# Performance work log

Measured on AMD Instinct MI355X. Metric: run time of the kernel, lower is better.

## Reference

```python
import jax, jax.numpy as jnp
import numpy as np

DIM, HID = 1024, 2048
N_SHARED, N_ROUTED, TOP_K = 2, 6, 2
AUX_W = 0.01
B, T = 4, 2048


def _swiglu(x, w1, w2, w3):
    # x: [N, C]; w1,w3: [C, H]; w2: [H, C]
    return (jax.nn.silu(x @ w1) * (x @ w3)) @ w2


def setup_inputs() -> dict:
    key = jax.random.key(0)
    ks = jax.random.split(key, 9)
    s = 0.02
    return {
        "x": jax.random.normal(ks[0], (B, T, DIM), dtype=jnp.float32),
        "w1_s": jax.random.normal(ks[1], (N_SHARED, DIM, HID), dtype=jnp.float32) * s,
        "w2_s": jax.random.normal(ks[2], (N_SHARED, HID, DIM), dtype=jnp.float32) * s,
        "w3_s": jax.random.normal(ks[3], (N_SHARED, DIM, HID), dtype=jnp.float32) * s,
        "w1_r": jax.random.normal(ks[4], (N_ROUTED, DIM, HID), dtype=jnp.float32) * s,
        "w2_r": jax.random.normal(ks[5], (N_ROUTED, HID, DIM), dtype=jnp.float32) * s,
        "w3_r": jax.random.normal(ks[6], (N_ROUTED, DIM, HID), dtype=jnp.float32) * s,
        "gate_w": jax.random.normal(ks[7], (DIM, N_ROUTED), dtype=jnp.float32) * s,
        "out_w": jax.random.normal(ks[8], (DIM, DIM), dtype=jnp.float32) * s,
    }


def reference(x, w1_s, w2_s, w3_s, w1_r, w2_r, w3_r, gate_w, out_w):
    Bv, Tv, C = x.shape
    xf = x.reshape(-1, C)  # [N, C]

    # shared experts: always run for every token
    shared = jnp.zeros_like(xf)
    for e in range(N_SHARED):
        shared = shared + _swiglu(xf, w1_s[e], w2_s[e], w3_s[e])

    # router
    logits = xf @ gate_w                       # [N, E]
    wk, idx = jax.lax.top_k(logits, TOP_K)     # [N, K]
    wk = jax.nn.softmax(wk, axis=-1)           # softmax over selected k only

    # routed experts: dense per-expert pass scaled by (zero for unselected) weight
    routed = jnp.zeros_like(xf)
    for e in range(N_ROUTED):
        we = jnp.sum(wk * (idx == e).astype(xf.dtype), axis=-1, keepdims=True)  # [N,1]
        routed = routed + we * _swiglu(xf, w1_r[e], w2_r[e], w3_r[e])

    combined = shared + routed

    # aux load-balance loss (top-1 assignment fraction x mean prob)
    probs = jax.nn.softmax(logits, axis=-1)
    f_i = jnp.mean(jax.nn.one_hot(idx[:, 0], N_ROUTED, dtype=xf.dtype), axis=0)
    p_i = jnp.mean(probs, axis=0)
    aux_loss = AUX_W * N_ROUTED * jnp.sum(f_i * p_i)

    out = (combined @ out_w).reshape(Bv, Tv, C)
    return out, aux_loss
```

## Files before the change

### kernel.cpp

```cpp
#include <hip/hip_runtime.h>
#include <hip/hip_bf16.h>
#include <cstdint>

#define DIMc 1024
#define HIDc 2048
#define NTOK 8192
#define NRT 6

typedef __bf16 bf16x8 __attribute__((ext_vector_type(8)));
typedef __bf16 bf16x2v __attribute__((ext_vector_type(2)));
typedef float  f32x4  __attribute__((ext_vector_type(4)));

#define VMCNT(n) asm volatile("s_waitcnt vmcnt(" #n ")" ::: "memory")
#define RBAR()   asm volatile("s_barrier" ::: "memory")

__device__ __forceinline__ void gl_lds16(const void* gsrc, void* ldst) {
    auto g = (const __attribute__((address_space(1))) void*)gsrc;
    auto l = (__attribute__((address_space(3))) void*)ldst;
    __builtin_amdgcn_global_load_lds(g, l, 16, 0, 0);
}

__device__ __forceinline__ void xcd_swz(int lid, int nwg, int gx, int& bx, int& by) {
    int q = nwg >> 3, r = nwg & 7;
    int xcd = lid & 7, idx = lid >> 3;
    int nlid = (xcd < r ? xcd * (q + 1) : r * (q + 1) + (xcd - r) * q) + idx;
    bx = nlid % gx; by = nlid / gx;
}

__global__ __launch_bounds__(256) void tcvt_k(
    const float* __restrict__ w1s, const float* __restrict__ w2s, const float* __restrict__ w3s,
    const float* __restrict__ w1r, const float* __restrict__ w2r, const float* __restrict__ w3r,
    const float* __restrict__ outw,
    __bf16* __restrict__ W13T, __bf16* __restrict__ W2T, __bf16* __restrict__ OutWT)
{
    int id = blockIdx.z;
    const float* src; __bf16* dst; int K, N; size_t S;
    if (id < 4) {
        int half = id >> 1, ex = id & 1;
        src = (half ? w3s : w1s) + (size_t)ex * DIMc * HIDc;
        K = 1024; N = 2048; S = 1024;
        dst = W13T + ((size_t)half * 4096 + ex * 2048) * 1024;
    } else if (id < 16) {
        int j = id - 4; int ex = j >> 1, half = j & 1;
        src = (half ? w3r : w1r) + (size_t)ex * DIMc * HIDc;
        K = 1024; N = 2048; S = 1024;
        dst = W13T + ((size_t)8192 + ex * 4096 + half * 2048) * 1024;
    } else if (id < 18) {
        int ex = id - 16;
        src = w2s + (size_t)ex * HIDc * DIMc;
        K = 2048; N = 1024; S = 4096;
        dst = W2T + ex * 2048;
    } else if (id < 24) {
        int ex = id - 18;
        src = w2r + (size_t)ex * HIDc * DIMc;
        K = 2048; N = 1024; S = 2048;
        dst = W2T + (size_t)4096 * 1024 + (size_t)ex * 2048 * 1024;
    } else {
        src = outw; K = 1024; N = 1024; S = 1024; dst = OutWT;
    }
    int n0 = blockIdx.x * 32, k0 = blockIdx.y * 32;
    if (n0 >= N || k0 >= K) return;
    __shared__ float t[32][33];
    int c = threadIdx.x & 31, rb = threadIdx.x >> 5;
#pragma unroll
    for (int i = 0; i < 4; i++) {
        int r = rb + i * 8;
        t[r][c] = src[(size_t)(k0 + r) * N + n0 + c];
    }
    __syncthreads();
    int kp = threadIdx.x & 15, nn = threadIdx.x >> 4;
#pragma unroll
    for (int pass = 0; pass < 2; pass++) {
        int n = nn + pass * 16;
        bf16x2v v; v[0] = (__bf16)t[2 * kp][n]; v[1] = (__bf16)t[2 * kp + 1][n];
        *(bf16x2v*)&dst[(size_t)(n0 + n) * S + k0 + 2 * kp] = v;
    }
}

__global__ __launch_bounds__(256) void router_k(
    const float* __restrict__ x, const float* __restrict__ gate,
    __bf16* __restrict__ xb, int* __restrict__ tke, float* __restrict__ tkw,
    float* __restrict__ auxp, float* __restrict__ auxf, int* __restrict__ rcnt)
{
    __shared__ float gl[DIMc * NRT];
    __shared__ float pacc[NRT];
    __shared__ int hist1[NRT], hist2[NRT];
    for (int i = threadIdx.x; i < DIMc * NRT; i += 256) gl[i] = gate[i];
    if (threadIdx.x < NRT) { pacc[threadIdx.x] = 0.f; hist1[threadIdx.x] = 0; hist2[threadIdx.x] = 0; }
    __syncthreads();
    int lane = threadIdx.x & 63, wid = threadIdx.x >> 6;
    for (int rep = 0; rep < 4; rep++) {
        int t = blockIdx.x * 16 + wid * 4 + rep;
        float a[NRT] = {0.f, 0.f, 0.f, 0.f, 0.f, 0.f};
        const float* xr = x + (size_t)t * DIMc;
        __bf16* xbr = xb + (size_t)t * DIMc;
        for (int k = lane; k < DIMc; k += 64) {
            float v = xr[k];
            xbr[k] = (__bf16)v;
#pragma unroll
            for (int e = 0; e < NRT; e++) a[e] += v * gl[k * NRT + e];
        }
#pragma unroll
        for (int e = 0; e < NRT; e++)
#pragma unroll
            for (int m = 32; m; m >>= 1) a[e] += __shfl_xor(a[e], m);
        if (lane == 0) {
            int i0 = 0; float m0 = a[0];
#pragma unroll
            for (int e = 1; e < NRT; e++) if (a[e] > m0) { m0 = a[e]; i0 = e; }
            int i1 = -1; float m1 = -1e30f;
#pragma unroll
            for (int e = 0; e < NRT; e++) if (e != i0 && a[e] > m1) { m1 = a[e]; i1 = e; }
            float w1 = __expf(m1 - m0);
            float inv = 1.f / (1.f + w1);
            tke[2 * t] = i0; tke[2 * t + 1] = i1;
            tkw[2 * t] = inv; tkw[2 * t + 1] = w1 * inv;
            float se = 0.f, pe[NRT];
#pragma unroll
            for (int e = 0; e < NRT; e++) { pe[e] = __expf(a[e] - m0); se += pe[e]; }
            float rinv = 1.f / se;
#pragma unroll
            for (int e = 0; e < NRT; e++) atomicAdd(&pacc[e], pe[e] * rinv);
            atomicAdd(&hist1[i0], 1);
            atomicAdd(&hist2[i0], 1); atomicAdd(&hist2[i1], 1);
        }
    }
    __syncthreads();
    if (threadIdx.x < NRT) {
        atomicAdd(&auxp[threadIdx.x], pacc[threadIdx.x]);
        atomicAdd(&auxf[threadIdx.x], (float)hist1[threadIdx.x]);
        atomicAdd(&rcnt[threadIdx.x], hist2[threadIdx.x]);
    }
}

__global__ void offsets_k(const int* __restrict__ rcnt, int* __restrict__ goff, int* __restrict__ gcnt) {
    if (threadIdx.x == 0) {
        int off = 0;
        for (int e = 0; e < NRT; e++) { goff[e] = off; gcnt[e] = rcnt[e]; off += rcnt[e]; }
    }
}

__global__ __launch_bounds__(256) void scatter_k(
    const int* __restrict__ tke, const float* __restrict__ tkw,
    const int* __restrict__ goff, int* __restrict__ curs,
    int* __restrict__ perm, float* __restrict__ wrow, int* __restrict__ islot)
{
    int t = blockIdx.x * 256 + threadIdx.x;
    if (t >= NTOK) return;
#pragma unroll
    for (int k = 0; k < 2; k++) {
        int e = tke[2 * t + k]; float w = tkw[2 * t + k];
        int slot = atomicAdd(&curs[e], 1);
        int sr = goff[e] + slot;
        perm[sr] = t; wrow[sr] = w; islot[2 * t + k] = sr;
    }
}

__global__ void auxfin_k(const float* __restrict__ auxp, const float* __restrict__ auxf, float* __restrict__ out) {
    if (threadIdx.x == 0) {
        float s = 0.f;
        for (int e = 0; e < NRT; e++) s += (auxf[e] * (1.f / NTOK)) * (auxp[e] * (1.f / NTOK));
        out[(size_t)NTOK * DIMc] = 0.01f * 6.f * s;
    }
}

template <int SHARED>
__global__ __launch_bounds__(512, 2) void gemm13_k(
    const __bf16* __restrict__ A, const __bf16* __restrict__ W13, __bf16* __restrict__ gbuf,
    const int* __restrict__ goff, const int* __restrict__ gcnt, const int* __restrict__ perm)
{
    __shared__ __bf16 lds[4 * 16384];
    int cnt, gofs, h3row, gstride;
    const __bf16* Bg;
    if constexpr (SHARED) {
        cnt = NTOK; gofs = 0; h3row = 4096; gstride = 4096; Bg = W13;
    } else {
        int e = blockIdx.z;
        cnt = gcnt[e]; gofs = goff[e]; h3row = 2048; gstride = 2048;
        Bg = W13 + ((size_t)8192 + (size_t)e * 4096) * 1024;
    }
    int bx, by;
    xcd_swz(blockIdx.x + gridDim.x * blockIdx.y, gridDim.x * gridDim.y, gridDim.x, bx, by);
    if (bx * 256 >= cnt) return;
    const int tid = threadIdx.x;
    const int lane = tid & 63, wid = tid >> 6;
    const int wr = wid >> 2, wc = wid & 3;
    const int l15 = lane & 15, l4 = lane >> 4;

    const __bf16* agA[2]; const __bf16* agB[2];
    int ldsA[2], ldsB[2];
#pragma unroll
    for (int i = 0; i < 2; i++) {
        int cA = i * 512 + tid;
        int rowA = cA >> 2, qA = cA & 3;
        int r = bx * 256 + rowA; if (r > cnt - 1) r = cnt - 1;
        size_t arow = SHARED ? (size_t)r : (size_t)perm[gofs + r];
        agA[i] = A + arow * 1024 + qA * 8;
        ldsA[i] = cA * 8;
        int cB = i * 512 + tid;
        int jr = cB >> 2, qB = cB & 3;
        int g = jr >> 5, s = jr & 31;
        int r1 = by * 128 + g * 16 + (s & 15);
        int brow = (s < 16) ? r1 : (h3row + r1);
        agB[i] = Bg + (size_t)brow * 1024 + qB * 8;
        ldsB[i] = cB * 8;
    }

#define STG13(slot, kt) { __bf16* d_ = lds + (slot) * 16384; \
    gl_lds16(agA[0] + (kt) * 32, d_ + ldsA[0]); \
    gl_lds16(agA[1] + (kt) * 32, d_ + ldsA[1]); \
    gl_lds16(agB[0] + (kt) * 32, d_ + 8192 + ldsB[0]); \
    gl_lds16(agB[1] + (kt) * 32, d_ + 8192 + ldsB[1]); }

    f32x4 acc[8][4];
#pragma unroll
    for (int mi = 0; mi < 8; mi++)
#pragma unroll
        for (int ni = 0; ni < 4; ni++)
#pragma unroll
            for (int j = 0; j < 4; j++) acc[mi][ni][j] = 0.f;

#define CMP13(slot) { \
    const __bf16* As = lds + (slot) * 16384; \
    const __bf16* Bs = As + 8192; \
    bf16x8 av[8], bv[4]; \
    _Pragma("unroll") for (int mi = 0; mi < 8; mi++) \
        av[mi] = *(const bf16x8*)&As[(wr * 128 + mi * 16 + l15) * 32 + l4 * 8]; \
    _Pragma("unroll") for (int ni = 0; ni < 4; ni++) \
        bv[ni] = *(const bf16x8*)&Bs[(wc * 64 + ni * 16 + l15) * 32 + l4 * 8]; \
    __builtin_amdgcn_s_setprio(1); \
    _Pragma("unroll") for (int mi = 0; mi < 8; mi++) \
        _Pragma("unroll") for (int ni = 0; ni < 4; ni++) \
            acc[mi][ni] = __builtin_amdgcn_mfma_f32_16x16x32_bf16(av[mi], bv[ni], acc[mi][ni], 0, 0, 0); \
    __builtin_amdgcn_s_setprio(0); }

    const int nkt = 32;
    STG13(0, 0); STG13(1, 1); STG13(2, 2);
    int kt = 0;
    for (; kt < nkt - 3; kt++) {
        VMCNT(8); RBAR();
        STG13((kt + 3) & 3, kt + 3);
        CMP13(kt & 3);
    }
    VMCNT(8); RBAR(); CMP13(kt & 3); kt++;
    VMCNT(4); RBAR(); CMP13(kt & 3); kt++;
    VMCNT(0); RBAR(); CMP13(kt & 3);

#pragma unroll
    for (int mi = 0; mi < 8; mi++) {
#pragma unroll
        for (int j = 0; j < 4; j++) {
            int r = bx * 256 + wr * 128 + mi * 16 + l4 * 4 + j;
            if (r < cnt) {
                size_t orow = (size_t)(gofs + r) * gstride;
#pragma unroll
                for (int p = 0; p < 2; p++) {
                    int c = by * 128 + wc * 32 + p * 16 + l15;
                    float h1 = acc[mi][2 * p][j], h3 = acc[mi][2 * p + 1][j];
                    float sg = h1 / (1.f + __expf(-h1));
                    gbuf[orow + c] = (__bf16)(sg * h3);
                }
            }
        }
    }
#undef STG13
#undef CMP13
}

template <int MODE>
__global__ __launch_bounds__(512, 2) void gemmNN_k(
    const __bf16* __restrict__ A, const __bf16* __restrict__ B,
    __bf16* __restrict__ outB16, float* __restrict__ outF32,
    const float* __restrict__ wrow, const int* __restrict__ goff, const int* __restrict__ gcnt,
    int K)
{
    __shared__ __bf16 lds[4 * 12288];
    int cnt, gofs;
    const __bf16* Bg;
    if constexpr (MODE == 1) {
        int e = blockIdx.z;
        cnt = gcnt[e]; gofs = goff[e];
        Bg = B + (size_t)e * 2048 * 1024;
    } else {
        cnt = NTOK; gofs = 0; Bg = B;
    }
    int bx, by;
    xcd_swz(blockIdx.x + gridDim.x * blockIdx.y, gridDim.x * gridDim.y, gridDim.x, bx, by);
    if (bx * 256 >= cnt) return;
    const int tid = threadIdx.x;
    const int lane = tid & 63, wid = tid >> 6;
    const int wr = wid >> 1, wc = wid & 1;
    const int l15 = lane & 15, l4 = lane >> 4;

    const __bf16* agA[2]; const __bf16* agB1;
    int ldsA[2], ldsB1;
#pragma unroll
    for (int i = 0; i < 2; i++) {
        int cA = i * 512 + tid;
        int rowA = cA >> 2, qA = cA & 3;
        int r = bx * 256 + rowA; if (r > cnt - 1) r = cnt - 1;
        agA[i] = A + (size_t)(gofs + r) * K + qA * 8;
        ldsA[i] = cA * 8;
    }
    {
        int cB = tid;
        int jr = cB >> 2, qB = cB & 3;
        agB1 = Bg + (size_t)(by * 128 + jr) * K + qB * 8;
        ldsB1 = cB * 8;
    }

#define STGNN(slot, kt) { __bf16* d_ = lds + (slot) * 12288; \
    gl_lds16(agA[0] + (kt) * 32, d_ + ldsA[0]); \
    gl_lds16(agA[1] + (kt) * 32, d_ + ldsA[1]); \
    gl_lds16(agB1 + (kt) * 32, d_ + 8192 + ldsB1); }

    f32x4 acc[4][4];
#pragma unroll
    for (int mi = 0; mi < 4; mi++)
#pragma unroll
        for (int ni = 0; ni < 4; ni++)
#pragma unroll
            for (int j = 0; j < 4; j++) acc[mi][ni][j] = 0.f;

#define CMPNN(slot) { \
    const __bf16* As = lds + (slot) * 12288; \
    const __bf16* Bs = As + 8192; \
    bf16x8 av[4], bv[4]; \
    _Pragma("unroll") for (int mi = 0; mi < 4; mi++) \
        av[mi] = *(const bf16x8*)&As[(wr * 64 + mi * 16 + l15) * 32 + l4 * 8]; \
    _Pragma("unroll") for (int ni = 0; ni < 4; ni++) \
        bv[ni] = *(const bf16x8*)&Bs[(wc * 64 + ni * 16 + l15) * 32 + l4 * 8]; \
    __builtin_amdgcn_s_setprio(1); \
    _Pragma("unroll") for (int mi = 0; mi < 4; mi++) \
        _Pragma("unroll") for (int ni = 0; ni < 4; ni++) \
            acc[mi][ni] = __builtin_amdgcn_mfma_f32_16x16x32_bf16(av[mi], bv[ni], acc[mi][ni], 0, 0, 0); \
    __builtin_amdgcn_s_setprio(0); }

    const int nkt = K >> 5;
    STGNN(0, 0); STGNN(1, 1); STGNN(2, 2);
    int kt = 0;
    for (; kt < nkt - 3; kt++) {
        VMCNT(6); RBAR();
        STGNN((kt + 3) & 3, kt + 3);
        CMPNN(kt & 3);
    }
    VMCNT(6); RBAR(); CMPNN(kt & 3); kt++;
    VMCNT(3); RBAR(); CMPNN(kt & 3); kt++;
    VMCNT(0); RBAR(); CMPNN(kt & 3);

#pragma unroll
    for (int mi = 0; mi < 4; mi++) {
#pragma unroll
        for (int j = 0; j < 4; j++) {
            int r = bx * 256 + wr * 64 + mi * 16 + l4 * 4 + j;
            if (r < cnt) {
                if constexpr (MODE == 0) {
                    size_t orow = (size_t)r * 1024;
#pragma unroll
                    for (int ni = 0; ni < 4; ni++) {
                        int c = by * 128 + wc * 64 + ni * 16 + l15;
                        outB16[orow + c] = (__bf16)acc[mi][ni][j];
                    }
                } else if constexpr (MODE == 1) {
                    int sr = gofs + r;
                    float w = wrow[sr];
                    size_t orow = (size_t)(8192 + sr) * 1024;
#pragma unroll
                    for (int ni = 0; ni < 4; ni++) {
                        int c = by * 128 + wc * 64 + ni * 16 + l15;
                        outB16[orow + c] = (__bf16)(w * acc[mi][ni][j]);
                    }
                } else {
                    size_t orow = (size_t)r * 1024;
#pragma unroll
                    for (int ni = 0; ni < 4; ni++) {
                        int c = by * 128 + wc * 64 + ni * 16 + l15;
                        outF32[orow + c] = acc[mi][ni][j];
                    }
                }
            }
        }
    }
#undef STGNN
#undef CMPNN
}

__global__ __launch_bounds__(256) void combine_k(
    const __bf16* __restrict__ ybuf, const int* __restrict__ islot, __bf16* __restrict__ cb)
{
    int tid = threadIdx.x;
    int row = blockIdx.x * 2 + (tid >> 7);
    int c8 = (tid & 127) * 8;
    int s0 = islot[2 * row], s1 = islot[2 * row + 1];
    bf16x8 vs = *(const bf16x8*)&ybuf[(size_t)row * 1024 + c8];
    bf16x8 v0 = *(const bf16x8*)&ybuf[(size_t)(8192 + s0) * 1024 + c8];
    bf16x8 v1 = *(const bf16x8*)&ybuf[(size_t)(8192 + s1) * 1024 + c8];
    bf16x8 o;
#pragma unroll
    for (int j = 0; j < 8; j++) o[j] = (__bf16)((float)vs[j] + (float)v0[j] + (float)v1[j]);
    *(bf16x8*)&cb[(size_t)row * 1024 + c8] = o;
}

extern "C" void kernel_launch(void* const* d_in, const int* in_sizes, int n_in,
                              void* d_out, int out_size, void* d_ws, size_t ws_size,
                              hipStream_t stream) {
    const float* x    = (const float*)d_in[0];
    const float* w1s  = (const float*)d_in[1];
    const float* w2s  = (const float*)d_in[2];
    const float* w3s  = (const float*)d_in[3];
    const float* w1r  = (const float*)d_in[4];
    const float* w2r  = (const float*)d_in[5];
    const float* w3r  = (const float*)d_in[6];
    const float* gate = (const float*)d_in[7];
    const float* outw = (const float*)d_in[8];
    float* out = (float*)d_out;

    char* ws = (char*)d_ws;
    float* auxp = (float*)ws;
    float* auxf = auxp + 8;
    int*   rcnt = (int*)(ws + 64);
    int*   curs = rcnt + 8;
    size_t off = 256;
    __bf16* xb    = (__bf16*)(ws + off); off += 16777216;
    __bf16* W13T  = (__bf16*)(ws + off); off += 67108864;
    __bf16* W2T   = (__bf16*)(ws + off); off += 33554432;
    __bf16* OutWT = (__bf16*)(ws + off); off += 2097152;
    __bf16* gbuf  = (__bf16*)(ws + off); off += 67108864;
    __bf16* cb    = gbuf;
    __bf16* ybuf  = (__bf16*)(ws + off); off += 50331648;
    int*   tke   = (int*)(ws + off);   off += 65536;
    float* tkw   = (float*)(ws + off); off += 65536;
    int*   perm  = (int*)(ws + off);   off += 65536;
    float* wrow  = (float*)(ws + off); off += 65536;
    int*   islot = (int*)(ws + off);   off += 65536;
    int*   goffp = (int*)(ws + off);   off += 64;
    int*   gcntp = (int*)(ws + off);   off += 64;

    hipMemsetAsync(d_ws, 0, 256, stream);

    dim3 b256(256), b512(512);
    tcvt_k<<<dim3(64, 64, 25), b256, 0, stream>>>(w1s, w2s, w3s, w1r, w2r, w3r, outw, W13T, W2T, OutWT);
    router_k<<<dim3(512), b256, 0, stream>>>(x, gate, xb, tke, tkw, auxp, auxf, rcnt);
    offsets_k<<<dim3(1), dim3(64), 0, stream>>>(rcnt, goffp, gcntp);
    scatter_k<<<dim3(32), b256, 0, stream>>>(tke, tkw, goffp, curs, perm, wrow, islot);
    auxfin_k<<<dim3(1), dim3(64), 0, stream>>>(auxp, auxf, out);

    gemm13_k<1><<<dim3(32, 32, 1), b512, 0, stream>>>(xb, W13T, gbuf, goffp, gcntp, perm);
    gemmNN_k<0><<<dim3(32, 8, 1), b512, 0, stream>>>(gbuf, W2T, ybuf, nullptr, wrow, goffp, gcntp, 4096);
    gemm13_k<0><<<dim3(32, 16, 6), b512, 0, stream>>>(xb, W13T, gbuf, goffp, gcntp, perm);
    gemmNN_k<1><<<dim3(64, 8, 6), b512, 0, stream>>>(gbuf, W2T + (size_t)4096 * 1024, ybuf, nullptr, wrow, goffp, gcntp, 2048);

    combine_k<<<dim3(4096), b256, 0, stream>>>(ybuf, islot, cb);
    gemmNN_k<2><<<dim3(32, 8, 1), b512, 0, stream>>>(cb, OutWT, nullptr, out, wrow, goffp, gcntp, 1024);
}
```

Measured before the change: 924.4 us.

## Retile GEMMs to BK=64 with XOR-swizzled LDS and 3-stage pipeline

Both GEMM kernels move from a K-tile of 32 with 4 LDS stages to a K-tile of 64 with 3 stages. LDS chunks are XOR-swizzled to avoid bank conflicts on the wider rows. The gate/up kernel narrows its N tile from 128 to 64, which doubles its grid and halves its accumulators. The down-projection kernel changes to 256x128 tiles with 8 waves. This is meant to cut barrier and sync count per FLOP and reduce LDS bank conflicts. It adds an extra barrier per iteration, and the larger LDS footprint (144KB per block) may limit occupancy.

```diff
diff --git a/kernel.cpp b/kernel.cpp
--- a/kernel.cpp
+++ b/kernel.cpp
@@ -169,7 +169,7 @@
     const __bf16* __restrict__ A, const __bf16* __restrict__ W13, __bf16* __restrict__ gbuf,
     const int* __restrict__ goff, const int* __restrict__ gcnt, const int* __restrict__ perm)
 {
-    __shared__ __bf16 lds[4 * 16384];
+    __shared__ __bf16 lds[3 * 24576];
     int cnt, gofs, h3row, gstride;
     const __bf16* Bg;
     if constexpr (SHARED) {
@@ -187,64 +187,74 @@
     const int wr = wid >> 2, wc = wid & 3;
     const int l15 = lane & 15, l4 = lane >> 4;
 
-    const __bf16* agA[2]; const __bf16* agB[2];
-    int ldsA[2], ldsB[2];
+    const __bf16* agA[4]; const __bf16* agB[2];
+    int ldsA[4], ldsB[2];
+#pragma unroll
+    for (int i = 0; i < 4; i++) {
+        int chunk = i * 512 + tid;
+        int row = chunk >> 3, cg = (chunk & 7) ^ (row & 7);
+        int r = bx * 256 + row; if (r > cnt - 1) r = cnt - 1;
+        size_t arow = SHARED ? (size_t)r : (size_t)perm[gofs + r];
+        agA[i] = A + arow * 1024 + cg * 8;
+        ldsA[i] = chunk * 8;
+    }
 #pragma unroll
     for (int i = 0; i < 2; i++) {
-        int cA = i * 512 + tid;
-        int rowA = cA >> 2, qA = cA & 3;
-        int r = bx * 256 + rowA; if (r > cnt - 1) r = cnt - 1;
-        size_t arow = SHARED ? (size_t)r : (size_t)perm[gofs + r];
-        agA[i] = A + arow * 1024 + qA * 8;
-        ldsA[i] = cA * 8;
-        int cB = i * 512 + tid;
-        int jr = cB >> 2, qB = cB & 3;
+        int chunk = i * 512 + tid;
+        int jr = chunk >> 3, cg = (chunk & 7) ^ (jr & 7);
         int g = jr >> 5, s = jr & 31;
-        int r1 = by * 128 + g * 16 + (s & 15);
-        int brow = (s < 16) ? r1 : (h3row + r1);
-        agB[i] = Bg + (size_t)brow * 1024 + qB * 8;
-        ldsB[i] = cB * 8;
-    }
-
-#define STG13(slot, kt) { __bf16* d_ = lds + (slot) * 16384; \
-    gl_lds16(agA[0] + (kt) * 32, d_ + ldsA[0]); \
-    gl_lds16(agA[1] + (kt) * 32, d_ + ldsA[1]); \
-    gl_lds16(agB[0] + (kt) * 32, d_ + 8192 + ldsB[0]); \
-    gl_lds16(agB[1] + (kt) * 32, d_ + 8192 + ldsB[1]); }
-
-    f32x4 acc[8][4];
+        int brow = (s < 16) ? (by * 64 + g * 16 + s) : (h3row + by * 64 + g * 16 + (s - 16));
+        agB[i] = Bg + (size_t)brow * 1024 + cg * 8;
+        ldsB[i] = chunk * 8;
+    }
+
+#define STG13(slot, kt) { __bf16* d_ = lds + (slot) * 24576; \
+    gl_lds16(agA[0] + (kt) * 64, d_ + ldsA[0]); \
+    gl_lds16(agA[1] + (kt) * 64, d_ + ldsA[1]); \
+    gl_lds16(agA[2] + (kt) * 64, d_ + ldsA[2]); \
+    gl_lds16(agA[3] + (kt) * 64, d_ + ldsA[3]); \
+    gl_lds16(agB[0] + (kt) * 64, d_ + 16384 + ldsB[0]); \
+    gl_lds16(agB[1] + (kt) * 64, d_ + 16384 + ldsB[1]); }
+
+    f32x4 acc[8][2];
 #pragma unroll
     for (int mi = 0; mi < 8; mi++)
 #pragma unroll
-        for (int ni = 0; ni < 4; ni++)
+        for (int ni = 0; ni < 2; ni++)
 #pragma unroll
             for (int j = 0; j < 4; j++) acc[mi][ni][j] = 0.f;
 
 #define CMP13(slot) { \
-    const __bf16* As = lds + (slot) * 16384; \
-    const __bf16* Bs = As + 8192; \
-    bf16x8 av[8], bv[4]; \
-    _Pragma("unroll") for (int mi = 0; mi < 8; mi++) \
-        av[mi] = *(const bf16x8*)&As[(wr * 128 + mi * 16 + l15) * 32 + l4 * 8]; \
-    _Pragma("unroll") for (int ni = 0; ni < 4; ni++) \
-        bv[ni] = *(const bf16x8*)&Bs[(wc * 64 + ni * 16 + l15) * 32 + l4 * 8]; \
-    __builtin_amdgcn_s_setprio(1); \
-    _Pragma("unroll") for (int mi = 0; mi < 8; mi++) \
-        _Pragma("unroll") for (int ni = 0; ni < 4; ni++) \
-            acc[mi][ni] = __builtin_amdgcn_mfma_f32_16x16x32_bf16(av[mi], bv[ni], acc[mi][ni], 0, 0, 0); \
-    __builtin_amdgcn_s_setprio(0); }
-
-    const int nkt = 32;
+    const __bf16* As = lds + (slot) * 24576; \
+    const __bf16* Bs = As + 16384; \
+    _Pragma("unroll") for (int kk = 0; kk < 2; kk++) { \
+        bf16x8 av[8], bv[2]; \
+        _Pragma("unroll") for (int mi = 0; mi < 8; mi++) { \
+            int lr = wr * 128 + mi * 16 + l15; \
+            int cr = (kk * 4 + l4) ^ (lr & 7); \
+            av[mi] = *(const bf16x8*)&As[lr * 64 + cr * 8]; } \
+        _Pragma("unroll") for (int ni = 0; ni < 2; ni++) { \
+            int jr = wc * 32 + ni * 16 + l15; \
+            int cr = (kk * 4 + l4) ^ (jr & 7); \
+            bv[ni] = *(const bf16x8*)&Bs[jr * 64 + cr * 8]; } \
+        __builtin_amdgcn_s_setprio(1); \
+        _Pragma("unroll") for (int mi = 0; mi < 8; mi++) \
+            _Pragma("unroll") for (int ni = 0; ni < 2; ni++) \
+                acc[mi][ni] = __builtin_amdgcn_mfma_f32_16x16x32_bf16(av[mi], bv[ni], acc[mi][ni], 0, 0, 0); \
+        __builtin_amdgcn_s_setprio(0); } }
+
+    const int nkt = 16;
     STG13(0, 0); STG13(1, 1); STG13(2, 2);
-    int kt = 0;
-    for (; kt < nkt - 3; kt++) {
-        VMCNT(8); RBAR();
-        STG13((kt + 3) & 3, kt + 3);
-        CMP13(kt & 3);
-    }
-    VMCNT(8); RBAR(); CMP13(kt & 3); kt++;
-    VMCNT(4); RBAR(); CMP13(kt & 3); kt++;
-    VMCNT(0); RBAR(); CMP13(kt & 3);
+    for (int kt = 0; kt < nkt; kt++) {
+        if (kt <= nkt - 3)      VMCNT(12);
+        else if (kt == nkt - 2) VMCNT(6);
+        else                    VMCNT(0);
+        RBAR();
+        int slot = kt % 3;
+        CMP13(slot);
+        RBAR();
+        if (kt + 3 < nkt) STG13(slot, kt + 3);
+    }
 
 #pragma unroll
     for (int mi = 0; mi < 8; mi++) {
@@ -253,13 +263,10 @@
             int r = bx * 256 + wr * 128 + mi * 16 + l4 * 4 + j;
             if (r < cnt) {
                 size_t orow = (size_t)(gofs + r) * gstride;
-#pragma unroll
-                for (int p = 0; p < 2; p++) {
-                    int c = by * 128 + wc * 32 + p * 16 + l15;
-                    float h1 = acc[mi][2 * p][j], h3 = acc[mi][2 * p + 1][j];
-                    float sg = h1 / (1.f + __expf(-h1));
-                    gbuf[orow + c] = (__bf16)(sg * h3);
-                }
+                int c = by * 64 + wc * 16 + l15;
+                float h1 = acc[mi][0][j], h3 = acc[mi][1][j];
+                float sg = h1 / (1.f + __expf(-h1));
+                gbuf[orow + c] = (__bf16)(sg * h3);
             }
         }
     }
@@ -274,7 +281,7 @@
     const float* __restrict__ wrow, const int* __restrict__ goff, const int* __restrict__ gcnt,
     int K)
 {
-    __shared__ __bf16 lds[4 * 12288];
+    __shared__ __bf16 lds[3 * 24576];
     int cnt, gofs;
     const __bf16* Bg;
     if constexpr (MODE == 1) {
@@ -289,76 +296,86 @@
     if (bx * 256 >= cnt) return;
     const int tid = threadIdx.x;
     const int lane = tid & 63, wid = tid >> 6;
-    const int wr = wid >> 1, wc = wid & 1;
+    const int wr = wid >> 2, wc = wid & 3;
     const int l15 = lane & 15, l4 = lane >> 4;
 
-    const __bf16* agA[2]; const __bf16* agB1;
-    int ldsA[2], ldsB1;
+    const __bf16* agA[4]; const __bf16* agB[2];
+    int ldsA[4], ldsB[2];
+#pragma unroll
+    for (int i = 0; i < 4; i++) {
+        int chunk = i * 512 + tid;
+        int row = chunk >> 3, cg = (chunk & 7) ^ (row & 7);
+        int r = bx * 256 + row; if (r > cnt - 1) r = cnt - 1;
+        agA[i] = A + (size_t)(gofs + r) * K + cg * 8;
+        ldsA[i] = chunk * 8;
+    }
 #pragma unroll
     for (int i = 0; i < 2; i++) {
-        int cA = i * 512 + tid;
-        int rowA = cA >> 2, qA = cA & 3;
-        int r = bx * 256 + rowA; if (r > cnt - 1) r = cnt - 1;
-        agA[i] = A + (size_t)(gofs + r) * K + qA * 8;
-        ldsA[i] = cA * 8;
-    }
-    {
-        int cB = tid;
-        int jr = cB >> 2, qB = cB & 3;
-        agB1 = Bg + (size_t)(by * 128 + jr) * K + qB * 8;
-        ldsB1 = cB * 8;
-    }
-
-#define STGNN(slot, kt) { __bf16* d_ = lds + (slot) * 12288; \
-    gl_lds16(agA[0] + (kt) * 32, d_ + ldsA[0]); \
-    gl_lds16(agA[1] + (kt) * 32, d_ + ldsA[1]); \
-    gl_lds16(agB1 + (kt) * 32, d_ + 8192 + ldsB1); }
-
-    f32x4 acc[4][4];
-#pragma unroll
-    for (int mi = 0; mi < 4; mi++)
-#pragma unroll
-        for (int ni = 0; ni < 4; ni++)
+        int chunk = i * 512 + tid;
+        int jr = chunk >> 3, cg = (chunk & 7) ^ (jr & 7);
+        agB[i] = Bg + (size_t)(by * 128 + jr) * K + cg * 8;
+        ldsB[i] = chunk * 8;
+    }
+
+#define STGNN(slot, kt) { __bf16* d_ = lds + (slot) * 24576; \
+    gl_lds16(agA[0] + (kt) * 64, d_ + ldsA[0]); \
+    gl_lds16(agA[1] + (kt) * 64, d_ + ldsA[1]); \
+    gl_lds16(agA[2] + (kt) * 64, d_ + ldsA[2]); \
+    gl_lds16(agA[3] + (kt) * 64, d_ + ldsA[3]); \
+    gl_lds16(agB[0] + (kt) * 64, d_ + 16384 + ldsB[0]); \
+    gl_lds16(agB[1] + (kt) * 64, d_ + 16384 + ldsB[1]); }
+
+    f32x4 acc[8][2];
+#pragma unroll
+    for (int mi = 0; mi < 8; mi++)
+#pragma unroll
+        for (int ni = 0; ni < 2; ni++)
 #pragma unroll
             for (int j = 0; j < 4; j++) acc[mi][ni][j] = 0.f;
 
 #define CMPNN(slot) { \
-    const __bf16* As = lds + (slot) * 12288; \
-    const __bf16* Bs = As + 8192; \
-    bf16x8 av[4], bv[4]; \
-    _Pragma("unroll") for (int mi = 0; mi < 4; mi++) \
-        av[mi] = *(const bf16x8*)&As[(wr * 64 + mi * 16 + l15) * 32 + l4 * 8]; \
-    _Pragma("unroll") for (int ni = 0; ni < 4; ni++) \
-        bv[ni] = *(const bf16x8*)&Bs[(wc * 64 + ni * 16 + l15) * 32 + l4 * 8]; \
-    __builtin_amdgcn_s_setprio(1); \
-    _Pragma("unroll") for (int mi = 0; mi < 4; mi++) \
-        _Pragma("unroll") for (int ni = 0; ni < 4; ni++) \
-            acc[mi][ni] = __builtin_amdgcn_mfma_f32_16x16x32_bf16(av[mi], bv[ni], acc[mi][ni], 0, 0, 0); \
-    __builtin_amdgcn_s_setprio(0); }
-
-    const int nkt = K >> 5;
+    const __bf16* As = lds + (slot) * 24576; \
+    const __bf16* Bs = As + 16384; \
+    _Pragma("unroll") for (int kk = 0; kk < 2; kk++) { \
+        bf16x8 av[8], bv[2]; \
+        _Pragma("unroll") for (int mi = 0; mi < 8; mi++) { \
+            int lr = wr * 128 + mi * 16 + l15; \
+            int cr = (kk * 4 + l4) ^ (lr & 7); \
+            av[mi] = *(const bf16x8*)&As[lr * 64 + cr * 8]; } \
+        _Pragma("unroll") for (int ni = 0; ni < 2; ni++) { \
+            int jr = wc * 32 + ni * 16 + l15; \
+            int cr = (kk * 4 + l4) ^ (jr & 7); \
+            bv[ni] = *(const bf16x8*)&Bs[jr * 64 + cr * 8]; } \
+        __builtin_amdgcn_s_setprio(1); \
+        _Pragma("unroll") for (int mi = 0; mi < 8; mi++) \
+            _Pragma("unroll") for (int ni = 0; ni < 2; ni++) \
+                acc[mi][ni] = __builtin_amdgcn_mfma_f32_16x16x32_bf16(av[mi], bv[ni], acc[mi][ni], 0, 0, 0); \
+        __builtin_amdgcn_s_setprio(0); } }
+
+    const int nkt = K >> 6;
     STGNN(0, 0); STGNN(1, 1); STGNN(2, 2);
-    int kt = 0;
-    for (; kt < nkt - 3; kt++) {
-        VMCNT(6); RBAR();
-        STGNN((kt + 3) & 3, kt + 3);
-        CMPNN(kt & 3);
-    }
-    VMCNT(6); RBAR(); CMPNN(kt & 3); kt++;
-    VMCNT(3); RBAR(); CMPNN(kt & 3); kt++;
-    VMCNT(0); RBAR(); CMPNN(kt & 3);
-
-#pragma unroll
-    for (int mi = 0; mi < 4; mi++) {
+    for (int kt = 0; kt < nkt; kt++) {
+        if (kt <= nkt - 3)      VMCNT(12);
+        else if (kt == nkt - 2) VMCNT(6);
+        else                    VMCNT(0);
+        RBAR();
+        int slot = kt % 3;
+        CMPNN(slot);
+        RBAR();
+        if (kt + 3 < nkt) STGNN(slot, kt + 3);
+    }
+
+#pragma unroll
+    for (int mi = 0; mi < 8; mi++) {
 #pragma unroll
         for (int j = 0; j < 4; j++) {
-            int r = bx * 256 + wr * 64 + mi * 16 + l4 * 4 + j;
+            int r = bx * 256 + wr * 128 + mi * 16 + l4 * 4 + j;
             if (r < cnt) {
                 if constexpr (MODE == 0) {
                     size_t orow = (size_t)r * 1024;
 #pragma unroll
-                    for (int ni = 0; ni < 4; ni++) {
-                        int c = by * 128 + wc * 64 + ni * 16 + l15;
+                    for (int ni = 0; ni < 2; ni++) {
+                        int c = by * 128 + wc * 32 + ni * 16 + l15;
                         outB16[orow + c] = (__bf16)acc[mi][ni][j];
                     }
                 } else if constexpr (MODE == 1) {
@@ -366,15 +383,15 @@
                     float w = wrow[sr];
                     size_t orow = (size_t)(8192 + sr) * 1024;
 #pragma unroll
-                    for (int ni = 0; ni < 4; ni++) {
-                        int c = by * 128 + wc * 64 + ni * 16 + l15;
+                    for (int ni = 0; ni < 2; ni++) {
+                        int c = by * 128 + wc * 32 + ni * 16 + l15;
                         outB16[orow + c] = (__bf16)(w * acc[mi][ni][j]);
                     }
                 } else {
                     size_t orow = (size_t)r * 1024;
 #pragma unroll
-                    for (int ni = 0; ni < 4; ni++) {
-                        int c = by * 128 + wc * 64 + ni * 16 + l15;
+                    for (int ni = 0; ni < 2; ni++) {
+                        int c = by * 128 + wc * 32 + ni * 16 + l15;
                         outF32[orow + c] = acc[mi][ni][j];
                     }
                 }
@@ -445,9 +462,9 @@
     scatter_k<<<dim3(32), b256, 0, stream>>>(tke, tkw, goffp, curs, perm, wrow, islot);
     auxfin_k<<<dim3(1), dim3(64), 0, stream>>>(auxp, auxf, out);
 
-    gemm13_k<1><<<dim3(32, 32, 1), b512, 0, stream>>>(xb, W13T, gbuf, goffp, gcntp, perm);
+    gemm13_k<1><<<dim3(32, 64, 1), b512, 0, stream>>>(xb, W13T, gbuf, goffp, gcntp, perm);
     gemmNN_k<0><<<dim3(32, 8, 1), b512, 0, stream>>>(gbuf, W2T, ybuf, nullptr, wrow, goffp, gcntp, 4096);
-    gemm13_k<0><<<dim3(32, 16, 6), b512, 0, stream>>>(xb, W13T, gbuf, goffp, gcntp, perm);
+    gemm13_k<0><<<dim3(64, 32, 6), b512, 0, stream>>>(xb, W13T, gbuf, goffp, gcntp, perm);
     gemmNN_k<1><<<dim3(64, 8, 6), b512, 0, stream>>>(gbuf, W2T + (size_t)4096 * 1024, ybuf, nullptr, wrow, goffp, gcntp, 2048);
 
     combine_k<<<dim3(4096), b256, 0, stream>>>(ybuf, islot, cb);
```

Result: slower. 1.008 ms (+9.1%).
